# Kernel optimization log

Hardware: AMD Instinct MI355X
Metric: run time of the kernel (lower is better)

The kernel has to match this reference:

```python
import math
import jax, jax.numpy as jnp
from jax import lax
import numpy as np

C = 256; A = 3; NIMG = 2; L = 5
SIZES = [(200, 304), (100, 152), (50, 76), (25, 38), (13, 19)]
STRIDES = [4, 8, 16, 32, 64]
LVTOP = 600          # cfg['lvtop'] (eval)
IMTOP = 300          # cfg['imtop1'] (eval)
SCORE_THR = 0.0      # cfg['score_thr1']
MIN_SIZE = 1e-2      # cfg['min_size1']
IOU_THR = 0.7        # cfg['iou_thr1']
IMH, IMW = 800.0, 1216.0
BBOX_CLIP = math.log(1000.0 / 16.0)   # clamp=True in decode_boxes
GROUP_OFF = 4096.0                     # > max canvas coord -> disjoint NMS groups


def _level_anchors(h, w, stride):
    scale = stride * 8.0
    r = np.array([0.5, 1.0, 2.0])
    ws = scale * np.sqrt(r); hs = scale / np.sqrt(r)          # [A]
    ys, xs = np.meshgrid(np.arange(h), np.arange(w), indexing='ij')
    cx = (xs.reshape(-1, 1) + 0.5) * stride                    # [HW,1]
    cy = (ys.reshape(-1, 1) + 0.5) * stride
    a = np.stack([cx - ws / 2, cy - hs / 2, cx + ws / 2, cy + hs / 2], axis=-1)
    return a.reshape(-1, 4).astype(np.float32)                 # [HW*A,4]


def setup_inputs() -> dict:
    key = jax.random.key(0)
    ks = jax.random.split(key, 10)
    inp = {}
    for i, (h, w) in enumerate(SIZES):
        inp[f'fmap{i}'] = jax.random.normal(ks[i], (NIMG, C, h, w), jnp.float32)
        inp[f'priors{i}'] = jnp.asarray(_level_anchors(h, w, STRIDES[i]))
    inp['imsizes'] = jnp.array([[IMH, IMW]] * NIMG, jnp.float32)   # (h, w) per image
    inp['conv_w'] = jax.random.normal(ks[5], (C, C, 3, 3), jnp.float32) * 0.03
    inp['conv_b'] = jnp.zeros((C,), jnp.float32)
    inp['log_w'] = jax.random.normal(ks[6], (A, C), jnp.float32) * 0.03
    inp['log_b'] = jnp.zeros((A,), jnp.float32)
    inp['reg_w'] = jax.random.normal(ks[7], (A * 4, C), jnp.float32) * 0.01
    inp['reg_b'] = jnp.zeros((A * 4,), jnp.float32)
    return inp


def _decode(reg, pri):
    pw = pri[..., 2] - pri[..., 0]; ph = pri[..., 3] - pri[..., 1]
    pcx = pri[..., 0] + 0.5 * pw;   pcy = pri[..., 1] + 0.5 * ph
    dx, dy = reg[..., 0], reg[..., 1]
    dw = jnp.minimum(reg[..., 2], BBOX_CLIP)
    dh = jnp.minimum(reg[..., 3], BBOX_CLIP)
    cx = dx * pw + pcx; cy = dy * ph + pcy
    w = pw * jnp.exp(dw); h = ph * jnp.exp(dh)
    return jnp.stack([cx - 0.5 * w, cy - 0.5 * h, cx + 0.5 * w, cy + 0.5 * h], axis=-1)


def _forward(fmaps, priors, imsizes, conv_w, conv_b, log_w, log_b, reg_w, reg_b):
    dn = ('NCHW', 'OIHW', 'NCHW')
    boxes_l, score_l = [], []
    for x, pri in zip(fmaps, priors):
        n = x.shape[0]
        h = jax.nn.relu(lax.conv_general_dilated(x, conv_w, (1, 1), 'SAME',
                                                 dimension_numbers=dn)
                        + conv_b[None, :, None, None])
        logit = (jnp.einsum('nchw,ac->nahw', h, log_w)
                 + log_b[None, :, None, None]).transpose(0, 2, 3, 1).reshape(n, -1)
        reg = (jnp.einsum('nchw,ac->nahw', h, reg_w)
               + reg_b[None, :, None, None]).transpose(0, 2, 3, 1).reshape(n, -1, 4)
        vals, top = lax.top_k(logit, LVTOP)                        # per-level topk
        reg_g = jnp.take_along_axis(reg, jnp.broadcast_to(top[:, :, None], (n, LVTOP, 4)), axis=1)
        pri_g = pri[top]                                           # [n,k,4]
        boxes_l.append(_decode(reg_g, pri_g))
        score_l.append(jax.nn.sigmoid(vals))
    boxes = jnp.concatenate(boxes_l, axis=1)                       # [n, L*k, 4]
    obj = jnp.concatenate(score_l, axis=1)                         # [n, L*k]
    n, dim = boxes.shape[0], boxes.shape[1]
    Nall = n * dim
    boxes = boxes.reshape(Nall, 4); obj = obj.reshape(Nall)
    imidx = jnp.arange(Nall) // dim
    lvl = jnp.tile(jnp.repeat(jnp.arange(L), LVTOP), n)
    valid = obj >= SCORE_THR
    sz = imsizes[imidx]                                            # [Nall,2] (h,w)
    boxes = jnp.stack([jnp.clip(boxes[:, 0], 0.0, sz[:, 1]),
                       jnp.clip(boxes[:, 1], 0.0, sz[:, 0]),
                       jnp.clip(boxes[:, 2], 0.0, sz[:, 1]),
                       jnp.clip(boxes[:, 3], 0.0, sz[:, 0])], axis=-1)
    valid = valid & (boxes[:, 2] - boxes[:, 0] >= MIN_SIZE) & (boxes[:, 3] - boxes[:, 1] >= MIN_SIZE)
    groups = imidx * 10 + lvl                                      # batched_nms groups
    # sort by score, invalid entries pushed to the end
    order = jnp.argsort(-jnp.where(valid, obj, -1.0))
    b = boxes[order]; v = valid[order]; g = groups[order]; im = imidx[order]
    # group-offset trick == torchvision batched_nms
    ob = b + g.astype(b.dtype)[:, None] * GROUP_OFF
    area = (ob[:, 2] - ob[:, 0]) * (ob[:, 3] - ob[:, 1])
    lt = jnp.maximum(ob[:, None, :2], ob[None, :, :2])
    rb = jnp.minimum(ob[:, None, 2:], ob[None, :, 2:])
    wh = jnp.maximum(rb - lt, 0.0)
    inter = wh[..., 0] * wh[..., 1]
    iou = lax.stop_gradient(inter / (area[:, None] + area[None, :] - inter))
    idxr = jnp.arange(Nall)
    def body(i, keep):
        sup = jnp.any(keep & (iou[i] > IOU_THR) & (idxr < i))
        return keep.at[i].set(v[i] & ~sup)
    keep = lax.fori_loop(0, Nall, body, jnp.zeros((Nall,), bool))
    # per-image cap at IMTOP (keep is already in score order)
    sel = keep[None, :] & (im[None, :] == jnp.arange(n)[:, None])  # [n,Nall]
    sel = sel & (jnp.cumsum(sel, axis=1) <= IMTOP)
    prio = jnp.where(sel, Nall - idxr[None, :], 0)
    pvals, pos = lax.top_k(prio, IMTOP)                            # [n,IMTOP]
    vout = pvals > 0
    bout = jnp.where(vout[..., None], b[pos], 0.0)                 # [n,IMTOP,4]
    imout = jnp.broadcast_to(jnp.arange(n)[:, None], (n, IMTOP)).reshape(-1).astype(jnp.int32)
    return bout.reshape(-1, 4), imout, vout.reshape(-1)


def reference(fmap0, fmap1, fmap2, fmap3, fmap4,
              priors0, priors1, priors2, priors3, priors4,
              imsizes, conv_w, conv_b, log_w, log_b, reg_w, reg_b):
    return _forward([fmap0, fmap1, fmap2, fmap3, fmap4],
                    [priors0, priors1, priors2, priors3, priors4],
                    imsizes, conv_w, conv_b, log_w, log_b, reg_w, reg_b)
```

## Files before the change

### kernel.cpp

```cpp
#include <hip/hip_runtime.h>
#include <math.h>

typedef unsigned long long u64;
typedef unsigned int u32;
typedef unsigned short u16;
typedef _Float16 f16;
typedef __attribute__((ext_vector_type(8))) _Float16 f16x8;
typedef __attribute__((ext_vector_type(8))) unsigned short ushort8;
typedef __attribute__((ext_vector_type(4))) float f32x4;

#define LVTOP 600
#define IMTOP 300
#define NIMG 2
#define NLVL 5
#define NCAND (NLVL*LVTOP)

__constant__ int d_HW[5]    = {60800,15200,3800,950,247};
__constant__ int d_LGOFF[5] = {0,364800,456000,478800,484500};
__constant__ int d_RGOFF[5] = {0,1459200,1824000,1915200,1938000};
__constant__ int d_H[5]  = {200,100,50,25,13};
__constant__ int d_W[5]  = {304,152,76,38,19};
__constant__ int d_TX[5] = {5,3,2,1,1};
__constant__ long d_XB[5] = {0, 31129600, 38912000, 40857600, 41344000};
__constant__ long d_CB[5] = {0, 3891200, 4864000, 5107200, 5168000};
__constant__ int d_SB[6] = {0,64,80,84,85,86};
#define NCHUNK 5183808
#define WS_NEED 178889200ull

__device__ __forceinline__ u32 okey(float f){
  u32 u = __float_as_uint(f);
  return (u & 0x80000000u) ? ~u : (u | 0x80000000u);
}

__device__ __forceinline__ void f16_split(float v, u16& hb, u16& lb){
  f16 h = (f16)v;
  float r = v - (float)h;
  f16 l = (f16)r;
  hb = __builtin_bit_cast(u16, h);
  lb = __builtin_bit_cast(u16, l);
}

__device__ __forceinline__ u64 shfl64(u64 v, int src){
  u32 lo = __shfl((u32)v, src);
  u32 hi = __shfl((u32)(v >> 32), src);
  return ((u64)hi << 32) | lo;
}

__device__ __forceinline__ void dma16(const u16* g, u16* l){
  __builtin_amdgcn_global_load_lds(
      (const __attribute__((address_space(1))) u32*)g,
      (__attribute__((address_space(3))) u32*)l, 16, 0, 0);
}

template<int NN, int NT>
__device__ void bitonic_desc64(u64* a, int tid){
  for (int k = 2; k <= NN; k <<= 1){
    for (int j = k >> 1; j > 0; j >>= 1){
      __syncthreads();
      for (int i = tid; i < NN; i += NT){
        int ixj = i ^ j;
        if (ixj > i){
          u64 x = a[i], y = a[ixj];
          bool up = ((i & k) == 0);
          if (up ? (x < y) : (x > y)){ a[i] = y; a[ixj] = x; }
        }
      }
    }
  }
  __syncthreads();
}

template<int NN, int NT>
__device__ void bitonic_asc32(u32* a, int tid){
  for (int k = 2; k <= NN; k <<= 1){
    for (int j = k >> 1; j > 0; j >>= 1){
      __syncthreads();
      for (int i = tid; i < NN; i += NT){
        int ixj = i ^ j;
        if (ixj > i){
          u32 x = a[i], y = a[ixj];
          bool up = ((i & k) == 0);
          if (up ? (x > y) : (x < y)){ a[i] = y; a[ixj] = x; }
        }
      }
    }
  }
  __syncthreads();
}

__device__ void suffix_scan(u32* s, int NB, int tid){
  for (int off = 1; off < NB; off <<= 1){
    u32 v0 = 0, v1 = 0;
    int i1 = tid + 1024;
    if (tid < NB) v0 = s[tid] + ((tid + off < NB) ? s[tid + off] : 0u);
    if (i1  < NB) v1 = s[i1]  + ((i1  + off < NB) ? s[i1  + off] : 0u);
    __syncthreads();
    if (tid < NB) s[tid] = v0;
    if (i1  < NB) s[i1]  = v1;
    __syncthreads();
  }
}

__global__ __launch_bounds__(256) void wprep(
    const float* __restrict__ cw, const float* __restrict__ lw,
    const float* __restrict__ rw, u16* __restrict__ wT, u16* __restrict__ whB,
    u32* __restrict__ ghist)
{
  int t = threadIdx.x;
  if (blockIdx.x < 72){
    int id = blockIdx.x*256 + t;
    int cc = id & 7;
    int co = (id >> 3) & 255;
    int tap = id >> 11;
    int ntg = co >> 4;
    size_t base = (size_t)((tap*8 + cc)*16 + ntg) * 1024;
    #pragma unroll
    for (int ci = 0; ci < 32; ci++){
      float v = cw[(size_t)co*2304 + (size_t)(cc*32 + ci)*9 + tap];
      u16 hi, lo; f16_split(v, hi, lo);
      int q = ci >> 3, j = ci & 7;
      int lane = q*16 + (co & 15);
      wT[base + lane*8 + j] = hi;
      wT[base + 512 + lane*8 + j] = lo;
    }
  } else if (blockIdx.x == 72){
    if (t < 128){
      int ks = t >> 4, nn = t & 15;
      for (int ci = 0; ci < 32; ci++){
        int k = ks*32 + ci;
        float v = 0.0f;
        if (nn < 3) v = lw[nn*256 + k];
        else if (nn < 15) v = rw[(nn-3)*256 + k];
        u16 hi, lo; f16_split(v, hi, lo);
        int q = ci >> 3, j = ci & 7;
        int lane = q*16 + nn;
        whB[ks*1024 + lane*8 + j] = hi;
        whB[ks*1024 + 512 + lane*8 + j] = lo;
      }
    }
  } else {
    int z = (blockIdx.x - 73)*1024 + t;
    #pragma unroll
    for (int q = 0; q < 4; q++){
      int i = z + q*256;
      if (i < NLVL*NIMG*2048) ghist[i] = 0;
    }
  }
}

__global__ __launch_bounds__(256) void xsplit(
    const float* __restrict__ f0, const float* __restrict__ f1,
    const float* __restrict__ f2, const float* __restrict__ f3,
    const float* __restrict__ f4,
    u16* __restrict__ xh, u16* __restrict__ xl, u16* __restrict__ zp)
{
  long id = (long)blockIdx.x*256 + threadIdx.x;
  if (blockIdx.x == 0 && threadIdx.x < 8) zp[threadIdx.x] = 0;
  if (id >= NCHUNK) return;
  int l = (id < d_CB[1]) ? 0 : (id < d_CB[2]) ? 1 : (id < d_CB[3]) ? 2 : (id < d_CB[4]) ? 3 : 4;
  long rem = id - d_CB[l];
  int HW = d_HW[l];
  int n = (int)(rem / (32*HW));
  int r2 = (int)(rem - (long)n*32*HW);
  int cg = r2 / HW;
  int p = r2 - cg*HW;
  const float* fm = (l==0)?f0:(l==1)?f1:(l==2)?f2:(l==3)?f3:f4;
  const float* gp = fm + ((size_t)(n*256 + cg*8))*HW + p;
  ushort8 hv, lv;
  #pragma unroll
  for (int j = 0; j < 8; j++){
    float v = gp[(size_t)j*HW];
    u16 hb, lb; f16_split(v, hb, lb);
    hv[j] = hb; lv[j] = lb;
  }
  *(ushort8*)&xh[id*8] = hv;
  *(ushort8*)&xl[id*8] = lv;
}

__global__ __launch_bounds__(256, 3) void conv_mfma(
    const float* __restrict__ f0, const float* __restrict__ f1,
    const float* __restrict__ f2, const float* __restrict__ f3,
    const float* __restrict__ f4,
    const u16* __restrict__ xh, const u16* __restrict__ xl,
    const u16* __restrict__ zp,
    const u16* __restrict__ wT, const u16* __restrict__ whB,
    const float* __restrict__ cb, const float* __restrict__ lb,
    const float* __restrict__ rb,
    float* __restrict__ lgb, float* __restrict__ rgb, int use_dma)
{
  __shared__ __align__(16) u16 smem[26624];

  const int t = threadIdx.x;
  const int n = blockIdx.y;
  int bx = blockIdx.x;
  int l, rbk;
  if (bx < 1000){ l = 0; rbk = bx; }
  else if (bx < 1300){ l = 1; rbk = bx - 1000; }
  else if (bx < 1400){ l = 2; rbk = bx - 1300; }
  else if (bx < 1425){ l = 3; rbk = bx - 1400; }
  else { l = 4; rbk = bx - 1425; }
  const int H = d_H[l], W = d_W[l], tilesX = d_TX[l];
  const int ty = rbk / tilesX;
  const int x0 = (rbk - ty*tilesX) * 64;
  const float* fm = (l==0) ? f0 : (l==1) ? f1 : (l==2) ? f2 : (l==3) ? f3 : f4;

  const int wave = t >> 6, lane = t & 63;
  const int quad = lane >> 4, l15 = lane & 15;
  const int HWp = H * W;
  const float* xin = fm + (size_t)n * 256 * HWp;

  f32x4 acc[4][4];
  #pragma unroll
  for (int a = 0; a < 4; a++)
    #pragma unroll
    for (int b = 0; b < 4; b++) acc[a][b] = (f32x4){0.f,0.f,0.f,0.f};

  auto compute_cc = [&](int cc, int bufo){
    const u16* btb = wT + (size_t)((cc*16) + wave*4) * 1024 + lane*8;
    f16x8 Bh = *(const f16x8*)(btb);
    f16x8 Bl = *(const f16x8*)(btb + 512);
    #pragma unroll
    for (int tap = 0; tap < 9; tap++){
      const int ky = tap / 3, kx = tap - ky*3;
      int o0 = bufo + ((quad*3 + ky)*68 + (l15 + kx))*8;
      f16x8 Ah[4], Al[4];
      #pragma unroll
      for (int mt = 0; mt < 4; mt++){
        Ah[mt] = *(const f16x8*)&smem[o0 + mt*128];
        Al[mt] = *(const f16x8*)&smem[o0 + 6656 + mt*128];
      }
      const u16* bt = btb + (size_t)tap * (8*16*1024);
      #pragma unroll
      for (int nt = 0; nt < 4; nt++){
        f16x8 cBh = Bh, cBl = Bl;
        const u16* np = (nt < 3) ? (bt + (nt+1)*1024)
                      : ((tap < 8) ? (bt + 8*16*1024) : bt);
        Bh = *(const f16x8*)np;
        Bl = *(const f16x8*)(np + 512);
        #pragma unroll
        for (int mt = 0; mt < 4; mt++){
          acc[mt][nt] = __builtin_amdgcn_mfma_f32_16x16x32_f16(Ah[mt], cBh, acc[mt][nt], 0,0,0);
          acc[mt][nt] = __builtin_amdgcn_mfma_f32_16x16x32_f16(Al[mt], cBh, acc[mt][nt], 0,0,0);
          acc[mt][nt] = __builtin_amdgcn_mfma_f32_16x16x32_f16(Ah[mt], cBl, acc[mt][nt], 0,0,0);
        }
      }
    }
  };

  if (use_dma){
    const u16* ph[4]; const u16* pl[4]; u32 pstep[4]; int dsth[4]; int kv[4];
    #pragma unroll
    for (int s = 0; s < 4; s++){
      int k = wave + s*4;
      kv[s] = (k < 13);
      int g = k*64 + lane;
      int gg = (g < 816) ? g : 0;
      int cg = gg / 204; int rem = gg - cg*204;
      int r = rem / 68;  int xi = rem - r*68;
      int gy = ty - 1 + r, gx = x0 - 1 + xi;
      bool inb = (g < 816) && (gy >= 0) && (gy < H) && (gx >= 0) && (gx < W);
      int gy2 = gy < 0 ? 0 : (gy >= H ? H-1 : gy);
      int gx2 = gx < 0 ? 0 : (gx >= W ? W-1 : gx);
      long off = d_XB[l] + (((long)(n*32 + cg))*HWp + (long)gy2*W + gx2)*8;
      ph[s] = inb ? (xh + off) : zp;
      pl[s] = inb ? (xl + off) : zp;
      pstep[s] = inb ? (u32)(32*HWp) : 0u;
      dsth[s] = k*512;
    }
    auto stage = [&](int bufo){
      #pragma unroll
      for (int s = 0; s < 4; s++){
        if (kv[s]){
          dma16(ph[s], &smem[bufo + dsth[s]]);
          dma16(pl[s], &smem[bufo + 6656 + dsth[s]]);
          ph[s] += pstep[s]; pl[s] += pstep[s];
        }
      }
    };
    stage(0);
    __syncthreads();
    for (int cc = 0; cc < 8; cc++){
      if (cc < 7) stage(((cc+1)&1)*13312);
      compute_cc(cc, (cc&1)*13312);
      __syncthreads();
    }
  } else {
    for (int cc = 0; cc < 8; cc++){
      __syncthreads();
      #pragma unroll
      for (int it = 0; it < 4; it++){
        int G = t + it*256;
        if (G < 816){
          int cg = G / 204; int rem = G - cg*204;
          int r = rem / 68; int xi = rem - r*68;
          int gy = ty - 1 + r, gx = x0 - 1 + xi;
          bool inb = (gy >= 0) & (gy < H) & (gx >= 0) & (gx < W);
          const float* gp = xin + (size_t)(cc*32 + cg*8) * HWp
                          + (size_t)(gy < 0 ? 0 : gy) * W + (gx < 0 ? 0 : gx);
          ushort8 hv, lv;
          #pragma unroll
          for (int j = 0; j < 8; j++){
            float v = inb ? gp[(size_t)j * HWp] : 0.0f;
            u16 hb, lb2; f16_split(v, hb, lb2);
            hv[j] = hb; lv[j] = lb2;
          }
          int off = ((cg*3 + r)*68 + xi)*8;
          *(ushort8*)&smem[off] = hv;
          *(ushort8*)&smem[6656 + off] = lv;
        }
      }
      __syncthreads();
      compute_cc(cc, 0);
    }
    __syncthreads();
  }

  u16* hA_h = smem;
  u16* hA_l = smem + 8704;
  f32x4 a2 = (f32x4){0.f,0.f,0.f,0.f};
  #pragma unroll
  for (int half = 0; half < 2; half++){
    if ((wave >> 1) == half){
      #pragma unroll
      for (int mt = 0; mt < 4; mt++){
        #pragma unroll
        for (int nt = 0; nt < 4; nt++){
          int col = (wave & 1)*64 + nt*16 + l15;
          float bias = cb[half*128 + col];
          #pragma unroll
          for (int r = 0; r < 4; r++){
            float h = fmaxf(acc[mt][nt][r] + bias, 0.0f);
            u16 hb, lb2; f16_split(h, hb, lb2);
            int pos = mt*16 + quad*4 + r;
            hA_h[pos*136 + col] = hb;
            hA_l[pos*136 + col] = lb2;
          }
        }
      }
    }
    __syncthreads();
    #pragma unroll
    for (int ks2 = 0; ks2 < 4; ks2++){
      int ks = half*4 + ks2;
      int ao = (wave*16 + l15)*136 + ks2*32 + quad*8;
      f16x8 Ah = *(const f16x8*)&hA_h[ao];
      f16x8 Al = *(const f16x8*)&hA_l[ao];
      const u16* wb = whB + ks*1024 + lane*8;
      f16x8 Bh = *(const f16x8*)wb;
      f16x8 Bl = *(const f16x8*)(wb + 512);
      a2 = __builtin_amdgcn_mfma_f32_16x16x32_f16(Ah, Bh, a2, 0,0,0);
      a2 = __builtin_amdgcn_mfma_f32_16x16x32_f16(Al, Bh, a2, 0,0,0);
      a2 = __builtin_amdgcn_mfma_f32_16x16x32_f16(Ah, Bl, a2, 0,0,0);
    }
    __syncthreads();
  }

  float* sm_out = (float*)smem;
  {
    int o = l15;
    float bias = (o < 3) ? lb[o] : ((o < 15) ? rb[o-3] : 0.0f);
    #pragma unroll
    for (int r = 0; r < 4; r++){
      int pos = wave*16 + quad*4 + r;
      sm_out[pos*16 + o] = a2[r] + bias;
    }
  }
  __syncthreads();
  {
    int P = W - x0; if (P > 64) P = 64;
    size_t pbase = (size_t)ty * W + x0;
    float* lg = lgb + d_LGOFF[l] + (size_t)n*HWp*3  + pbase*3;
    float* rg = rgb + d_RGOFF[l] + (size_t)n*HWp*12 + pbase*12;
    for (int j = t; j < P*3; j += 256)  lg[j] = sm_out[(j/3)*16 + (j%3)];
    for (int j = t; j < P*12; j += 256) rg[j] = sm_out[(j/12)*16 + 3 + (j%12)];
  }
}

__global__ __launch_bounds__(256) void hist1(
    const float* __restrict__ lg, u32* __restrict__ ghist)
{
  __shared__ u32 lh[2048];
  int t = threadIdx.x;
  int b = blockIdx.x, n = blockIdx.y;
  int l = (b < d_SB[1]) ? 0 : (b < d_SB[2]) ? 1 : (b < d_SB[3]) ? 2 : (b < d_SB[4]) ? 3 : 4;
  int s = b - d_SB[l], nsl = d_SB[l+1] - d_SB[l];
  int N = d_HW[l] * 3;
  const float* lgl = lg + d_LGOFF[l] + (size_t)n * N;
  for (int i = t; i < 2048; i += 256) lh[i] = 0;
  __syncthreads();
  int lo = (int)((long)N * s / nsl), hi = (int)((long)N * (s+1) / nsl);
  for (int i = lo + t; i < hi; i += 256)
    atomicAdd(&lh[okey(lgl[i]) >> 21], 1u);
  __syncthreads();
  u32* gh = ghist + (size_t)(l*NIMG + n) * 2048;
  for (int i = t; i < 2048; i += 256)
    if (lh[i]) atomicAdd(&gh[i], lh[i]);
}

__global__ __launch_bounds__(1024) void topk_decode(
    const float* __restrict__ lg, const float* __restrict__ rg,
    const float* __restrict__ pr0, const float* __restrict__ pr1,
    const float* __restrict__ pr2, const float* __restrict__ pr3,
    const float* __restrict__ pr4,
    const float* __restrict__ imsizes, const u32* __restrict__ ghist,
    float* __restrict__ cbox, float* __restrict__ cscore, u32* __restrict__ cvalid)
{
  __shared__ u32 hist[2048];
  __shared__ u32 sscan[2048];
  __shared__ u64 sel[1024];
  __shared__ u32 eqbuf[1024];
  __shared__ u32 scal[8];
  int tid = threadIdx.x;
  int l = blockIdx.x / NIMG;
  int n = blockIdx.x - l*NIMG;
  int HW = d_HW[l];
  int N = HW * 3;
  const float* lgl = lg + d_LGOFF[l] + (size_t)n * N;

  {
    const u32* gh = ghist + (size_t)blockIdx.x * 2048;
    for (int i = tid; i < 2048; i += 1024){ u32 h = gh[i]; hist[i] = h; sscan[i] = h; }
  }
  __syncthreads();
  suffix_scan(sscan, 2048, tid);
  if (tid < 2048){
    u32 Si = sscan[tid], Sn = (tid+1 < 2048) ? sscan[tid+1] : 0u;
    if (Si >= LVTOP && Sn < LVTOP){ scal[0] = (u32)tid; scal[1] = Si - hist[tid]; }
  }
  { int i2 = tid + 1024;
    u32 Si = sscan[i2], Sn = (i2+1 < 2048) ? sscan[i2+1] : 0u;
    if (Si >= LVTOP && Sn < LVTOP){ scal[0] = (u32)i2; scal[1] = Si - hist[i2]; } }
  __syncthreads();
  u32 B1 = scal[0], base1 = scal[1];

  for (int i = tid; i < 2048; i += 1024) hist[i] = 0;
  __syncthreads();
  for (int i = tid; i < N; i += 1024){
    u32 k = okey(lgl[i]);
    if ((k >> 21) == B1) atomicAdd(&hist[(k >> 10) & 0x7FFu], 1u);
  }
  __syncthreads();
  for (int i = tid; i < 2048; i += 1024) sscan[i] = hist[i];
  __syncthreads();
  suffix_scan(sscan, 2048, tid);
  {
    u32 need = LVTOP - base1;
    if (tid < 2048){
      u32 Si = sscan[tid], Sn = (tid+1 < 2048) ? sscan[tid+1] : 0u;
      if (Si >= need && Sn < need){ scal[2] = (u32)tid; scal[3] = base1 + Si - hist[tid]; }
    }
    int i2 = tid + 1024;
    u32 Si = sscan[i2], Sn = (i2+1 < 2048) ? sscan[i2+1] : 0u;
    if (Si >= need && Sn < need){ scal[2] = (u32)i2; scal[3] = base1 + Si - hist[i2]; }
  }
  __syncthreads();
  u32 B2 = scal[2], base2 = scal[3];

  for (int i = tid; i < 1024; i += 1024) hist[i] = 0;
  __syncthreads();
  u32 hi21 = (B1 << 11) | B2;
  for (int i = tid; i < N; i += 1024){
    u32 k = okey(lgl[i]);
    if ((k >> 10) == hi21) atomicAdd(&hist[k & 0x3FFu], 1u);
  }
  __syncthreads();
  for (int i = tid; i < 1024; i += 1024) sscan[i] = hist[i];
  __syncthreads();
  suffix_scan(sscan, 1024, tid);
  {
    u32 need = LVTOP - base2;
    if (tid < 1024){
      u32 Si = sscan[tid], Sn = (tid+1 < 1024) ? sscan[tid+1] : 0u;
      if (Si >= need && Sn < need){
        scal[4] = (hi21 << 10) | (u32)tid;
        scal[5] = base2 + Si - hist[tid];
      }
    }
  }
  if (tid == 0){ scal[6] = 0; scal[7] = 0; }
  __syncthreads();
  u32 T = scal[4], nAbove = scal[5], needEq = LVTOP - scal[5];

  for (int i = tid; i < 1024; i += 1024) sel[i] = 0;
  __syncthreads();
  for (int i = tid; i < N; i += 1024){
    u32 k = okey(lgl[i]);
    if (k > T){
      u32 p = atomicAdd(&scal[6], 1u);
      sel[p] = ((u64)k << 32) | (0xFFFFFFFFu - (u32)i);
    } else if (k == T){
      u32 p = atomicAdd(&scal[7], 1u);
      if (p < 1024) eqbuf[p] = (u32)i;
    }
  }
  __syncthreads();
  u32 cntE = scal[7];
  if (cntE > needEq){
    u32 m = cntE < 1024u ? cntE : 1024u;
    for (int i = tid; i < 1024; i += 1024) if ((u32)i >= m) eqbuf[i] = 0xFFFFFFFFu;
    __syncthreads();
    bitonic_asc32<1024,1024>(eqbuf, tid);
  }
  __syncthreads();
  if ((u32)tid < needEq)
    sel[nAbove + tid] = ((u64)T << 32) | (0xFFFFFFFFu - eqbuf[tid]);
  __syncthreads();
  bitonic_desc64<1024,1024>(sel, tid);

  if (tid < LVTOP){
    u64 c = sel[tid];
    u32 i = 0xFFFFFFFFu - (u32)c;
    float val = lgl[i];
    float score = 1.0f / (1.0f + expf(-val));
    int pp = (int)i / 3, a = (int)i - pp*3;
    const float* pri;
    if (l == 0) pri = pr0; else if (l == 1) pri = pr1; else if (l == 2) pri = pr2;
    else if (l == 3) pri = pr3; else pri = pr4;
    pri += (size_t)i * 4;
    const float* rgp = rg + d_RGOFF[l] + ((size_t)n * HW + pp) * 12 + a * 4;
    float px0 = pri[0], py0 = pri[1], px1 = pri[2], py1 = pri[3];
    float pw = px1 - px0, ph = py1 - py0;
    float pcx = px0 + 0.5f*pw, pcy = py0 + 0.5f*ph;
    const float BC = (float)4.135166556742356;
    float dx = rgp[0], dy = rgp[1];
    float dw = fminf(rgp[2], BC), dh = fminf(rgp[3], BC);
    float cx = dx*pw + pcx, cy = dy*ph + pcy;
    float bw = pw * expf(dw), bh = ph * expf(dh);
    float x1 = cx - 0.5f*bw, y1 = cy - 0.5f*bh;
    float x2 = cx + 0.5f*bw, y2 = cy + 0.5f*bh;
    float imh = imsizes[n*2+0], imw = imsizes[n*2+1];
    x1 = fminf(fmaxf(x1, 0.0f), imw);
    y1 = fminf(fmaxf(y1, 0.0f), imh);
    x2 = fminf(fmaxf(x2, 0.0f), imw);
    y2 = fminf(fmaxf(y2, 0.0f), imh);
    u32 valid = (score >= 0.0f) && ((x2 - x1) >= 1e-2f) && ((y2 - y1) >= 1e-2f);
    int ci = n*NCAND + l*LVTOP + tid;
    cbox[ci*4+0] = x1; cbox[ci*4+1] = y1; cbox[ci*4+2] = x2; cbox[ci*4+3] = y2;
    cscore[ci] = score; cvalid[ci] = valid;
  }
}

__global__ __launch_bounds__(1024) void sort_cand(
    const float* __restrict__ cscore, const u32* __restrict__ cvalid,
    const float* __restrict__ cbox,
    float* __restrict__ sbox, float* __restrict__ sob,
    float* __restrict__ sarea, u32* __restrict__ svalid,
    u32* __restrict__ rlist, u32* __restrict__ kflag)
{
  __shared__ u64 a[4096];
  int tid = threadIdx.x, n = blockIdx.x;
  for (int i = tid; i < 4096; i += 1024){
    if (i < NCAND){
      int ci = n*NCAND + i;
      float s = cvalid[ci] ? cscore[ci] : -1.0f;
      a[i] = ((u64)okey(s) << 32) | (0xFFFFFFFFu - (u32)i);
    } else a[i] = 0;
  }
  bitonic_desc64<4096,1024>(a, tid);
  int mylvl[3];
  #pragma unroll
  for (int q = 0; q < 3; q++){
    int r = tid + q*1024;
    mylvl[q] = 0;
    if (r < NCAND){
      u32 li = 0xFFFFFFFFu - (u32)a[r];
      int ci = n*NCAND + (int)li;
      float b0 = cbox[ci*4+0], b1 = cbox[ci*4+1], b2 = cbox[ci*4+2], b3 = cbox[ci*4+3];
      int lvl = (int)li / LVTOP;
      mylvl[q] = lvl;
      float off = (float)(n*10 + lvl) * 4096.0f;
      int so = n*NCAND + r;
      sbox[so*4+0]=b0; sbox[so*4+1]=b1; sbox[so*4+2]=b2; sbox[so*4+3]=b3;
      float o0=b0+off, o1=b1+off, o2=b2+off, o3=b3+off;
      sob[so*4+0]=o0; sob[so*4+1]=o1; sob[so*4+2]=o2; sob[so*4+3]=o3;
      sarea[so] = (o2-o0)*(o3-o1);
      svalid[so] = cvalid[ci];
    }
  }
  __syncthreads();
  #pragma unroll
  for (int q = 0; q < 3; q++){
    int r = tid + q*1024;
    a[r] = (r < NCAND) ? (1ull << (12*mylvl[q])) : 0ull;
  }
  a[tid + 3072] = 0ull;
  __syncthreads();
  for (int off = 1; off < 4096; off <<= 1){
    u64 v[4];
    #pragma unroll
    for (int q = 0; q < 4; q++){
      int i = tid + q*1024;
      v[q] = a[i] + ((i >= off) ? a[i-off] : 0ull);
    }
    __syncthreads();
    #pragma unroll
    for (int q = 0; q < 4; q++) a[tid + q*1024] = v[q];
    __syncthreads();
  }
  #pragma unroll
  for (int q = 0; q < 3; q++){
    int r = tid + q*1024;
    if (r < NCAND){
      int lv = mylvl[q];
      int pos = (int)((a[r] >> (12*lv)) & 0xFFFull) - 1;
      rlist[(n*NLVL + lv)*LVTOP + pos] = (u32)r;
      kflag[n*NCAND + r] = 0u;
    }
  }
}

__global__ __launch_bounds__(256) void nms_mask_l(
    const float* __restrict__ sob, const float* __restrict__ sarea,
    const u32* __restrict__ svalid, const u32* __restrict__ rlist,
    u64* __restrict__ pmask)
{
  __shared__ float sj[64*5];
  int tid = threadIdx.x;
  int nl = blockIdx.y;
  int n = nl / NLVL;
  int i = blockIdx.x*256 + tid;
  bool act = false;
  float oi0=0, oi1=0, oi2=0, oi3=0, ai=0;
  if (i < LVTOP){
    int so = n*NCAND + (int)rlist[nl*LVTOP + i];
    act = svalid[so] != 0;
    oi0 = sob[so*4+0]; oi1 = sob[so*4+1]; oi2 = sob[so*4+2]; oi3 = sob[so*4+3];
    ai = sarea[so];
  }
  for (int w = 0; w < 10; w++){
    __syncthreads();
    if (tid < 64){
      int j = w*64 + tid;
      if (j < LVTOP){
        int so = n*NCAND + (int)rlist[nl*LVTOP + j];
        sj[tid*5+0]=sob[so*4+0]; sj[tid*5+1]=sob[so*4+1];
        sj[tid*5+2]=sob[so*4+2]; sj[tid*5+3]=sob[so*4+3];
        sj[tid*5+4]=sarea[so];
      }
    }
    __syncthreads();
    if (act){
      u64 bits = 0;
      int jj0 = (i >= w*64) ? (i - w*64 + 1) : 0;
      int jjend = (LVTOP - w*64 < 64) ? (LVTOP - w*64) : 64;
      for (int jj = jj0; jj < jjend; jj++){
        float oj0=sj[jj*5+0], oj1=sj[jj*5+1], oj2=sj[jj*5+2], oj3=sj[jj*5+3], aj=sj[jj*5+4];
        float ltx = fmaxf(oi0, oj0), lty = fmaxf(oi1, oj1);
        float rbx = fminf(oi2, oj2), rby = fminf(oi3, oj3);
        float wx = fmaxf(rbx - ltx, 0.0f), wy = fmaxf(rby - lty, 0.0f);
        float inter = wx * wy;
        float iou = inter / ((ai + aj) - inter);
        if (iou > 0.7f) bits |= (1ull << jj);
      }
      pmask[((size_t)(nl*LVTOP + i))*10 + w] = bits;
    }
  }
}

__global__ __launch_bounds__(256) void nms_scan_l(
    const u64* __restrict__ pmask, const u32* __restrict__ svalid,
    const u32* __restrict__ rlist, u32* __restrict__ kflag)
{
  __shared__ u64 pm[LVTOP*10];
  int t = threadIdx.x, nl = blockIdx.x, n = nl / NLVL;
  const u64* gpm = pmask + (size_t)nl * LVTOP * 10;
  for (int i = t; i < LVTOP*10; i += 256) pm[i] = gpm[i];
  __syncthreads();
  if (t < 64){
    u64 vw = 0, remv = 0;
    for (int c = 0; c < 10; c++){
      int i = c*64 + t;
      int pred = 0;
      if (i < LVTOP) pred = svalid[n*NCAND + (int)rlist[nl*LVTOP + i]] != 0;
      u64 b = __ballot(pred);
      if (t == c) vw = b;
    }
    for (int w = 0; w < 10; w++){
      u64 act = shfl64(vw, w) & ~shfl64(remv, w);
      while (act){
        int bpos = __builtin_ctzll(act);
        int i = w*64 + bpos;
        if (t == 0) kflag[n*NCAND + (int)rlist[nl*LVTOP + i]] = 1u;
        u64 m = (t < 10) ? pm[i*10 + t] : 0ull;
        u64 mw = pm[i*10 + w];
        remv |= m;
        act &= ~(1ull << bpos);
        act &= ~mw;
      }
    }
  }
}

__global__ __launch_bounds__(1024) void merge_out(
    const u32* __restrict__ kflag, const float* __restrict__ sbox,
    float* __restrict__ out)
{
  __shared__ u32 ps[4096];
  int tid = threadIdx.x, n = blockIdx.x;
  u32 f[4];
  #pragma unroll
  for (int q = 0; q < 4; q++){
    int i = tid + q*1024;
    f[q] = (i < NCAND) ? kflag[n*NCAND + i] : 0u;
    ps[i] = f[q];
  }
  __syncthreads();
  for (int off = 1; off < 4096; off <<= 1){
    u32 v[4];
    #pragma unroll
    for (int q = 0; q < 4; q++){
      int i = tid + q*1024;
      v[q] = ps[i] + ((i >= off) ? ps[i-off] : 0u);
    }
    __syncthreads();
    #pragma unroll
    for (int q = 0; q < 4; q++) ps[tid + q*1024] = v[q];
    __syncthreads();
  }
  #pragma unroll
  for (int q = 0; q < 4; q++){
    int i = tid + q*1024;
    if (i < NCAND && f[q] && ps[i] <= IMTOP){
      int slot = n*IMTOP + (int)ps[i] - 1;
      int so = n*NCAND + i;
      out[slot*4+0] = sbox[so*4+0]; out[slot*4+1] = sbox[so*4+1];
      out[slot*4+2] = sbox[so*4+2]; out[slot*4+3] = sbox[so*4+3];
    }
  }
  u32 kept = ps[NCAND-1]; if (kept > IMTOP) kept = IMTOP;
  for (int j = tid; j < IMTOP; j += 1024){
    int slot = n*IMTOP + j;
    if ((u32)j >= kept){
      out[slot*4+0]=0; out[slot*4+1]=0; out[slot*4+2]=0; out[slot*4+3]=0;
    }
    out[2400 + slot] = (float)n;
    out[3000 + slot] = ((u32)j < kept) ? 1.0f : 0.0f;
  }
}

extern "C" void kernel_launch(void* const* d_in, const int* in_sizes, int n_in,
                              void* d_out, int out_size, void* d_ws, size_t ws_size,
                              hipStream_t stream)
{
  const float* fmap[5]   = {(const float*)d_in[0], (const float*)d_in[2], (const float*)d_in[4],
                            (const float*)d_in[6], (const float*)d_in[8]};
  const float* priors[5] = {(const float*)d_in[1], (const float*)d_in[3], (const float*)d_in[5],
                            (const float*)d_in[7], (const float*)d_in[9]};
  const float* imsz   = (const float*)d_in[10];
  const float* conv_w = (const float*)d_in[11];
  const float* conv_b = (const float*)d_in[12];
  const float* log_w  = (const float*)d_in[13];
  const float* log_b  = (const float*)d_in[14];
  const float* reg_w  = (const float*)d_in[15];
  const float* reg_b  = (const float*)d_in[16];

  char* base = (char*)d_ws;
  float* lg     = (float*)(base + 0);
  float* rg     = (float*)(base + 1943928);
  float* cscore = (float*)(base + 9719640);
  float* cbox   = (float*)(base + 9743640);
  u32*   cvalid = (u32*)  (base + 9839640);
  float* sbox   = (float*)(base + 9863640);
  float* sob    = (float*)(base + 9959640);
  float* sarea  = (float*)(base + 10055640);
  u32*   svalid = (u32*)  (base + 10079640);
  u32*   rlist  = (u32*)  (base + 10103640);
  u32*   kflag  = (u32*)  (base + 10127640);
  u64*   pmask  = (u64*)  (base + 10151648);
  u32*   ghist  = (u32*)  (base + 10151648);
  u16*   wT     = (u16*)  (base + 10631648);
  u16*   whB    = (u16*)  (base + 12990944);
  u16*   zp     = (u16*)  (base + 13007328);
  u16*   xh     = (u16*)  (base + 13007344);
  u16*   xl     = (u16*)  (base + 95948272);

  int use_dma = (ws_size >= WS_NEED) ? 1 : 0;

  wprep<<<93, 256, 0, stream>>>(conv_w, log_w, reg_w, wT, whB, ghist);
  if (use_dma)
    xsplit<<<(NCHUNK + 255)/256, 256, 0, stream>>>(
        fmap[0], fmap[1], fmap[2], fmap[3], fmap[4], xh, xl, zp);

  conv_mfma<<<dim3(1438, NIMG), 256, 0, stream>>>(
      fmap[0], fmap[1], fmap[2], fmap[3], fmap[4],
      xh, xl, zp, wT, whB, conv_b, log_b, reg_b, lg, rg, use_dma);

  hist1<<<dim3(86, NIMG), 256, 0, stream>>>(lg, ghist);

  topk_decode<<<NLVL*NIMG, 1024, 0, stream>>>(lg, rg,
      priors[0], priors[1], priors[2], priors[3], priors[4],
      imsz, ghist, cbox, cscore, cvalid);
  sort_cand<<<NIMG, 1024, 0, stream>>>(cscore, cvalid, cbox, sbox, sob, sarea,
                                       svalid, rlist, kflag);
  nms_mask_l<<<dim3(3, NIMG*NLVL), 256, 0, stream>>>(sob, sarea, svalid, rlist, pmask);
  nms_scan_l<<<NIMG*NLVL, 256, 0, stream>>>(pmask, svalid, rlist, kflag);
  merge_out<<<NIMG, 1024, 0, stream>>>(kflag, sbox, (float*)d_out);
}
```

Before: 1.212 ms.

## Retile conv to 2 output rows by 48 columns per block for weight reuse

Each conv block now computes two output rows of 48 pixels instead of one row of 64. Every weight fragment loaded from global memory is reused across both rows, and the halo overhead per output pixel drops. The accumulators grow to 2x3x4 tiles, so the occupancy hint falls from 3 to 2 blocks per CU. The grid shrinks accordingly and the epilogue loops over the two rows, guarding a partial last row.

```diff
diff --git a/kernel.cpp b/kernel.cpp
--- a/kernel.cpp
+++ b/kernel.cpp
@@ -20,7 +20,7 @@
 __constant__ int d_RGOFF[5] = {0,1459200,1824000,1915200,1938000};
 __constant__ int d_H[5]  = {200,100,50,25,13};
 __constant__ int d_W[5]  = {304,152,76,38,19};
-__constant__ int d_TX[5] = {5,3,2,1,1};
+__constant__ int d_TX[5] = {7,4,2,1,1};
 __constant__ long d_XB[5] = {0, 31129600, 38912000, 40857600, 41344000};
 __constant__ long d_CB[5] = {0, 3891200, 4864000, 5107200, 5168000};
 __constant__ int d_SB[6] = {0,64,80,84,85,86};
@@ -177,7 +177,7 @@
   *(ushort8*)&xl[id*8] = lv;
 }
 
-__global__ __launch_bounds__(256, 3) void conv_mfma(
+__global__ __launch_bounds__(256, 2) void conv_mfma(
     const float* __restrict__ f0, const float* __restrict__ f1,
     const float* __restrict__ f2, const float* __restrict__ f3,
     const float* __restrict__ f4,
@@ -194,14 +194,14 @@
   const int n = blockIdx.y;
   int bx = blockIdx.x;
   int l, rbk;
-  if (bx < 1000){ l = 0; rbk = bx; }
-  else if (bx < 1300){ l = 1; rbk = bx - 1000; }
-  else if (bx < 1400){ l = 2; rbk = bx - 1300; }
-  else if (bx < 1425){ l = 3; rbk = bx - 1400; }
-  else { l = 4; rbk = bx - 1425; }
+  if (bx < 700){ l = 0; rbk = bx; }
+  else if (bx < 900){ l = 1; rbk = bx - 700; }
+  else if (bx < 950){ l = 2; rbk = bx - 900; }
+  else if (bx < 963){ l = 3; rbk = bx - 950; }
+  else { l = 4; rbk = bx - 963; }
   const int H = d_H[l], W = d_W[l], tilesX = d_TX[l];
-  const int ty = rbk / tilesX;
-  const int x0 = (rbk - ty*tilesX) * 64;
+  const int ty2 = rbk / tilesX;
+  const int x0 = (rbk - ty2*tilesX) * 48;
   const float* fm = (l==0) ? f0 : (l==1) ? f1 : (l==2) ? f2 : (l==3) ? f3 : f4;
 
   const int wave = t >> 6, lane = t & 63;
@@ -209,39 +209,44 @@
   const int HWp = H * W;
   const float* xin = fm + (size_t)n * 256 * HWp;
 
-  f32x4 acc[4][4];
+  f32x4 acc[2][3][4];
   #pragma unroll
-  for (int a = 0; a < 4; a++)
+  for (int r = 0; r < 2; r++)
     #pragma unroll
-    for (int b = 0; b < 4; b++) acc[a][b] = (f32x4){0.f,0.f,0.f,0.f};
+    for (int a = 0; a < 3; a++)
+      #pragma unroll
+      for (int b = 0; b < 4; b++) acc[r][a][b] = (f32x4){0.f,0.f,0.f,0.f};
 
   auto compute_cc = [&](int cc, int bufo){
-    const u16* btb = wT + (size_t)((cc*16) + wave*4) * 1024 + lane*8;
-    f16x8 Bh = *(const f16x8*)(btb);
-    f16x8 Bl = *(const f16x8*)(btb + 512);
     #pragma unroll
-    for (int tap = 0; tap < 9; tap++){
-      const int ky = tap / 3, kx = tap - ky*3;
-      int o0 = bufo + ((quad*3 + ky)*68 + (l15 + kx))*8;
-      f16x8 Ah[4], Al[4];
+    for (int ky = 0; ky < 3; ky++){
       #pragma unroll
-      for (int mt = 0; mt < 4; mt++){
-        Ah[mt] = *(const f16x8*)&smem[o0 + mt*128];
-        Al[mt] = *(const f16x8*)&smem[o0 + 6656 + mt*128];
-      }
-      const u16* bt = btb + (size_t)tap * (8*16*1024);
-      #pragma unroll
-      for (int nt = 0; nt < 4; nt++){
-        f16x8 cBh = Bh, cBl = Bl;
-        const u16* np = (nt < 3) ? (bt + (nt+1)*1024)
-                      : ((tap < 8) ? (bt + 8*16*1024) : bt);
-        Bh = *(const f16x8*)np;
-        Bl = *(const f16x8*)(np + 512);
+      for (int kx = 0; kx < 3; kx++){
+        const u16* bt = wT + (size_t)((((ky*3+kx)*8 + cc)*16) + wave*4) * 1024 + lane*8;
+        f16x8 Bh[4], Bl[4];
         #pragma unroll
-        for (int mt = 0; mt < 4; mt++){
-          acc[mt][nt] = __builtin_amdgcn_mfma_f32_16x16x32_f16(Ah[mt], cBh, acc[mt][nt], 0,0,0);
-          acc[mt][nt] = __builtin_amdgcn_mfma_f32_16x16x32_f16(Al[mt], cBh, acc[mt][nt], 0,0,0);
-          acc[mt][nt] = __builtin_amdgcn_mfma_f32_16x16x32_f16(Ah[mt], cBl, acc[mt][nt], 0,0,0);
+        for (int nt = 0; nt < 4; nt++){
+          Bh[nt] = *(const f16x8*)(bt + nt*1024);
+          Bl[nt] = *(const f16x8*)(bt + nt*1024 + 512);
+        }
+        #pragma unroll
+        for (int row = 0; row < 2; row++){
+          int o0 = bufo + ((quad*4 + ky + row)*52 + (l15 + kx))*8;
+          f16x8 Ah[3], Al[3];
+          #pragma unroll
+          for (int mt = 0; mt < 3; mt++){
+            Ah[mt] = *(const f16x8*)&smem[o0 + mt*128];
+            Al[mt] = *(const f16x8*)&smem[o0 + 6656 + mt*128];
+          }
+          #pragma unroll
+          for (int nt = 0; nt < 4; nt++){
+            #pragma unroll
+            for (int mt = 0; mt < 3; mt++){
+              acc[row][mt][nt] = __builtin_amdgcn_mfma_f32_16x16x32_f16(Ah[mt], Bh[nt], acc[row][mt][nt], 0,0,0);
+              acc[row][mt][nt] = __builtin_amdgcn_mfma_f32_16x16x32_f16(Al[mt], Bh[nt], acc[row][mt][nt], 0,0,0);
+              acc[row][mt][nt] = __builtin_amdgcn_mfma_f32_16x16x32_f16(Ah[mt], Bl[nt], acc[row][mt][nt], 0,0,0);
+            }
+          }
         }
       }
     }
@@ -253,19 +258,19 @@
     for (int s = 0; s < 4; s++){
       int k = wave + s*4;
       kv[s] = (k < 13);
-      int g = k*64 + lane;
-      int gg = (g < 816) ? g : 0;
-      int cg = gg / 204; int rem = gg - cg*204;
-      int r = rem / 68;  int xi = rem - r*68;
-      int gy = ty - 1 + r, gx = x0 - 1 + xi;
-      bool inb = (g < 816) && (gy >= 0) && (gy < H) && (gx >= 0) && (gx < W);
+      int kk = kv[s] ? k : 0;
+      int g = kk*64 + lane;
+      int cg = g / 208; int rem = g - cg*208;
+      int r = rem / 52;  int xi = rem - r*52;
+      int gy = ty2*2 - 1 + r, gx = x0 - 1 + xi;
+      bool inb = (gy >= 0) && (gy < H) && (gx >= 0) && (gx < W);
       int gy2 = gy < 0 ? 0 : (gy >= H ? H-1 : gy);
       int gx2 = gx < 0 ? 0 : (gx >= W ? W-1 : gx);
       long off = d_XB[l] + (((long)(n*32 + cg))*HWp + (long)gy2*W + gx2)*8;
       ph[s] = inb ? (xh + off) : zp;
       pl[s] = inb ? (xl + off) : zp;
       pstep[s] = inb ? (u32)(32*HWp) : 0u;
-      dsth[s] = k*512;
+      dsth[s] = kk*512;
     }
     auto stage = [&](int bufo){
       #pragma unroll
@@ -290,10 +295,10 @@
       #pragma unroll
       for (int it = 0; it < 4; it++){
         int G = t + it*256;
-        if (G < 816){
-          int cg = G / 204; int rem = G - cg*204;
-          int r = rem / 68; int xi = rem - r*68;
-          int gy = ty - 1 + r, gx = x0 - 1 + xi;
+        if (G < 832){
+          int cg = G / 208; int rem = G - cg*208;
+          int r = rem / 52; int xi = rem - r*52;
+          int gy = ty2*2 - 1 + r, gx = x0 - 1 + xi;
           bool inb = (gy >= 0) & (gy < H) & (gx >= 0) & (gx < W);
           const float* gp = xin + (size_t)(cc*32 + cg*8) * HWp
                           + (size_t)(gy < 0 ? 0 : gy) * W + (gx < 0 ? 0 : gx);
@@ -304,7 +309,7 @@
             u16 hb, lb2; f16_split(v, hb, lb2);
             hv[j] = hb; lv[j] = lb2;
           }
-          int off = ((cg*3 + r)*68 + xi)*8;
+          int off = G*8;
           *(ushort8*)&smem[off] = hv;
           *(ushort8*)&smem[6656 + off] = lv;
         }
@@ -317,62 +322,70 @@
 
   u16* hA_h = smem;
   u16* hA_l = smem + 8704;
-  f32x4 a2 = (f32x4){0.f,0.f,0.f,0.f};
   #pragma unroll
-  for (int half = 0; half < 2; half++){
-    if ((wave >> 1) == half){
+  for (int row = 0; row < 2; row++){
+    const int ty = ty2*2 + row;
+    const bool rowok = (ty < H);
+    if (rowok){
+      f32x4 a2 = (f32x4){0.f,0.f,0.f,0.f};
       #pragma unroll
-      for (int mt = 0; mt < 4; mt++){
-        #pragma unroll
-        for (int nt = 0; nt < 4; nt++){
-          int col = (wave & 1)*64 + nt*16 + l15;
-          float bias = cb[half*128 + col];
+      for (int half = 0; half < 2; half++){
+        if ((wave >> 1) == half){
           #pragma unroll
-          for (int r = 0; r < 4; r++){
-            float h = fmaxf(acc[mt][nt][r] + bias, 0.0f);
-            u16 hb, lb2; f16_split(h, hb, lb2);
-            int pos = mt*16 + quad*4 + r;
-            hA_h[pos*136 + col] = hb;
-            hA_l[pos*136 + col] = lb2;
+          for (int mt = 0; mt < 3; mt++){
+            #pragma unroll
+            for (int nt = 0; nt < 4; nt++){
+              int col = (wave & 1)*64 + nt*16 + l15;
+              float bias = cb[half*128 + col];
+              #pragma unroll
+              for (int r = 0; r < 4; r++){
+                float h = fmaxf(acc[row][mt][nt][r] + bias, 0.0f);
+                u16 hb, lb2; f16_split(h, hb, lb2);
+                int pos = mt*16 + quad*4 + r;
+                hA_h[pos*136 + col] = hb;
+                hA_l[pos*136 + col] = lb2;
+              }
+            }
           }
         }
-      }
-    }
-    __syncthreads();
-    #pragma unroll
-    for (int ks2 = 0; ks2 < 4; ks2++){
-      int ks = half*4 + ks2;
-      int ao = (wave*16 + l15)*136 + ks2*32 + quad*8;
-      f16x8 Ah = *(const f16x8*)&hA_h[ao];
-      f16x8 Al = *(const f16x8*)&hA_l[ao];
-      const u16* wb = whB + ks*1024 + lane*8;
-      f16x8 Bh = *(const f16x8*)wb;
-      f16x8 Bl = *(const f16x8*)(wb + 512);
-      a2 = __builtin_amdgcn_mfma_f32_16x16x32_f16(Ah, Bh, a2, 0,0,0);
-      a2 = __builtin_amdgcn_mfma_f32_16x16x32_f16(Al, Bh, a2, 0,0,0);
-      a2 = __builtin_amdgcn_mfma_f32_16x16x32_f16(Ah, Bl, a2, 0,0,0);
-    }
-    __syncthreads();
-  }
-
-  float* sm_out = (float*)smem;
-  {
-    int o = l15;
-    float bias = (o < 3) ? lb[o] : ((o < 15) ? rb[o-3] : 0.0f);
-    #pragma unroll
-    for (int r = 0; r < 4; r++){
-      int pos = wave*16 + quad*4 + r;
-      sm_out[pos*16 + o] = a2[r] + bias;
-    }
-  }
-  __syncthreads();
-  {
-    int P = W - x0; if (P > 64) P = 64;
-    size_t pbase = (size_t)ty * W + x0;
-    float* lg = lgb + d_LGOFF[l] + (size_t)n*HWp*3  + pbase*3;
-    float* rg = rgb + d_RGOFF[l] + (size_t)n*HWp*12 + pbase*12;
-    for (int j = t; j < P*3; j += 256)  lg[j] = sm_out[(j/3)*16 + (j%3)];
-    for (int j = t; j < P*12; j += 256) rg[j] = sm_out[(j/12)*16 + 3 + (j%12)];
+        __syncthreads();
+        #pragma unroll
+        for (int ks2 = 0; ks2 < 4; ks2++){
+          int ks = half*4 + ks2;
+          int ao = (wave*16 + l15)*136 + ks2*32 + quad*8;
+          f16x8 Ah = *(const f16x8*)&hA_h[ao];
+          f16x8 Al = *(const f16x8*)&hA_l[ao];
+          const u16* wb = whB + ks*1024 + lane*8;
+          f16x8 Bh = *(const f16x8*)wb;
+          f16x8 Bl = *(const f16x8*)(wb + 512);
+          a2 = __builtin_amdgcn_mfma_f32_16x16x32_f16(Ah, Bh, a2, 0,0,0);
+          a2 = __builtin_amdgcn_mfma_f32_16x16x32_f16(Al, Bh, a2, 0,0,0);
+          a2 = __builtin_amdgcn_mfma_f32_16x16x32_f16(Ah, Bl, a2, 0,0,0);
+        }
+        __syncthreads();
+      }
+
+      float* sm_out = (float*)smem;
+      {
+        int o = l15;
+        float bias = (o < 3) ? lb[o] : ((o < 15) ? rb[o-3] : 0.0f);
+        #pragma unroll
+        for (int r = 0; r < 4; r++){
+          int pos = wave*16 + quad*4 + r;
+          sm_out[pos*16 + o] = a2[r] + bias;
+        }
+      }
+      __syncthreads();
+      {
+        int P = W - x0; if (P > 48) P = 48;
+        size_t pbase = (size_t)ty * W + x0;
+        float* lg = lgb + d_LGOFF[l] + (size_t)n*HWp*3  + pbase*3;
+        float* rg = rgb + d_RGOFF[l] + (size_t)n*HWp*12 + pbase*12;
+        for (int j = t; j < P*3; j += 256)  lg[j] = sm_out[(j/3)*16 + (j%3)];
+        for (int j = t; j < P*12; j += 256) rg[j] = sm_out[(j/12)*16 + 3 + (j%12)];
+      }
+      __syncthreads();
+    }
   }
 }
 
@@ -781,7 +794,7 @@
     xsplit<<<(NCHUNK + 255)/256, 256, 0, stream>>>(
         fmap[0], fmap[1], fmap[2], fmap[3], fmap[4], xh, xl, zp);
 
-  conv_mfma<<<dim3(1438, NIMG), 256, 0, stream>>>(
+  conv_mfma<<<dim3(970, NIMG), 256, 0, stream>>>(
       fmap[0], fmap[1], fmap[2], fmap[3], fmap[4],
       xh, xl, zp, wT, whB, conv_b, log_b, reg_b, lg, rg, use_dma);
 
```

Measured after the change: 1.118 ms. -7.8%, faster.
